# Kernel tuning notes

Hardware: AMD Instinct MI355X
Metric: run time of the kernel (lower is better)

## Reference

```python
import jax, jax.numpy as jnp
import numpy as np

B, J, H, W, P = 48, 17, 128, 128, 30  # batch, joints, heatmap HxW, max people
N = J * H * W  # flattened tag-map length per image


def setup_inputs() -> dict:
    key = jax.random.key(0)
    k1, k2, k3, k4 = jax.random.split(key, 4)
    outputs = jax.random.normal(k1, (B, 2 * J, H, W), dtype=jnp.float32)
    heatmaps = jax.random.uniform(k2, (B, J, H, W), dtype=jnp.float32)
    idx = jax.random.randint(k3, (B, P, J), 0, N)
    vis = jax.random.randint(k4, (B, P, J), 0, 2)
    joints = jnp.stack([idx, vis], axis=-1).astype(jnp.int64)  # [B,P,J,2]
    return {"outputs": outputs, "heatmaps": heatmaps, "joints": joints}


def _heatmap_mse(pred, gt):
    # mask over (batch, channel): channels whose gt sums to > 0
    mask = (gt.sum(axis=(2, 3)) > 0).astype(pred.dtype)  # [B,C]
    per = ((pred - gt) ** 2).mean(axis=(2, 3))            # [B,C]
    return (per * mask).sum() / mask.sum()


def _ae_loss(tags, joints):
    # tags: [B,N] flattened tag maps; joints: [B,P,J,2] int (idx, visibility)
    idx = joints[..., 0]
    vis = (joints[..., 1] > 0).astype(tags.dtype)         # [B,P,J]
    t = jax.vmap(lambda tg, ix: tg[ix])(tags, idx)        # [B,P,J] gathered tags
    cnt = vis.sum(-1)                                     # [B,P] visible joints per person
    person_valid = cnt > 0
    safe_cnt = jnp.where(person_valid, cnt, 1.0)
    m = (t * vis).sum(-1) / safe_cnt                      # [B,P] per-person mean tag
    per_pull = (vis * (t - m[..., None]) ** 2).sum(-1) / safe_cnt
    per_pull = jnp.where(person_valid, per_pull, 0.0)
    num_tags = person_valid.sum(-1).astype(tags.dtype)    # [B]
    pull = per_pull.sum(-1) / jnp.maximum(num_tags, 1.0)
    # push: all-pairs exp(-(m_i - m_j)^2) over valid persons, minus diagonal (num_tags)
    diff = m[:, :, None] - m[:, None, :]                  # [B,P,P]
    pair_mask = person_valid[:, :, None] & person_valid[:, None, :]
    push_raw = jnp.where(pair_mask, jnp.exp(-diff ** 2), 0.0).sum(axis=(1, 2)) - num_tags
    denom = (num_tags - 1.0) * num_tags
    push = jnp.where(num_tags >= 2.0,
                     push_raw / jnp.where(denom > 0, denom, 1.0) * 0.5,
                     0.0)
    return push, pull


def reference(outputs, heatmaps, joints):
    hm_pred = outputs[:, :J]                   # [B,J,H,W]
    tags = outputs[:, J:].reshape(B, -1)       # [B,N] (tag channels flattened)
    hm_loss = _heatmap_mse(hm_pred, heatmaps)  # scalar (factor 1.0)
    push, pull = _ae_loss(tags, joints)        # [B], [B] (factors 1.0)
    return hm_loss, push, pull
```

## Files before the change

### kernel.cpp

```cpp
#include <hip/hip_runtime.h>
#include <hip/hip_bf16.h>

constexpr int B = 48, J = 17, H = 128, W = 128, P = 30;
constexpr int HW = H * W;
constexpr int NPLANES = B * J;
constexpr int CHUNKS_PER_PLANE = 2;
constexpr int NCHUNK = NPLANES * CHUNKS_PER_PLANE;
constexpr int CHUNK_FLOATS = HW / CHUNKS_PER_PLANE;

__global__ __launch_bounds__(256) void fused_kernel(
        const float* __restrict__ outputs,
        const float* __restrict__ heatmaps,
        const unsigned* __restrict__ joints_u32,
        float* __restrict__ ws,
        float* __restrict__ out) {
    int t = threadIdx.x;

    if (blockIdx.x < NCHUNK) {
        int chunk = blockIdx.x;
        int plane = chunk >> 1, half = chunk & 1;
        int b = plane / J, j = plane % J;
        const float4* pred = reinterpret_cast<const float4*>(
            outputs + ((size_t)b * 2 * J + j) * HW + half * CHUNK_FLOATS);
        const float4* gt = reinterpret_cast<const float4*>(
            heatmaps + (size_t)plane * HW + half * CHUNK_FLOATS);

        float sq = 0.f, gs = 0.f;
#pragma unroll
        for (int k = 0; k < CHUNK_FLOATS / 4 / 256; ++k) {
            float4 p = pred[t + k * 256];
            float4 g = gt[t + k * 256];
            float d0 = p.x - g.x, d1 = p.y - g.y, d2 = p.z - g.z, d3 = p.w - g.w;
            sq += d0 * d0 + d1 * d1 + d2 * d2 + d3 * d3;
            gs += g.x + g.y + g.z + g.w;
        }
        for (int off = 32; off > 0; off >>= 1) {
            sq += __shfl_xor(sq, off);
            gs += __shfl_xor(gs, off);
        }
        __shared__ float s_sq[4], s_gs[4];
        int wave = t >> 6;
        if ((t & 63) == 0) { s_sq[wave] = sq; s_gs[wave] = gs; }
        __syncthreads();
        if (t == 0) {
            ws[2 * chunk]     = s_sq[0] + s_sq[1] + s_sq[2] + s_sq[3];
            ws[2 * chunk + 1] = s_gs[0] + s_gs[1] + s_gs[2] + s_gs[3];
        }
        return;
    }

    int b = blockIdx.x - NCHUNK;
    const float* tags = outputs + ((size_t)b * 2 * J + J) * HW;

    const unsigned* jw = joints_u32 + (size_t)b * P * J * 2 * 2;
    unsigned ob = 0;
#pragma unroll
    for (int k = 0; k < 4; ++k) {
        int i = t + k * 256;
        if (i < P * J * 2) ob |= jw[2 * i + 1];
    }
    __shared__ unsigned s_ob[4];
    for (int off = 32; off > 0; off >>= 1) ob |= (unsigned)__shfl_xor((int)ob, off);
    int wv = t >> 6;
    if ((t & 63) == 0) s_ob[wv] = ob;
    __shared__ float m_sh[P];
    __shared__ int v_sh[P];
    __syncthreads();
    bool is64 = (s_ob[0] | s_ob[1] | s_ob[2] | s_ob[3]) == 0u;

    if (t >= 64) return;
    int lane = t;

    float per_pull = 0.f, m = 0.f;
    int validp = 0;

    if (lane < P) {
        float tv[J];
        int   vv[J];
        int cnt = 0;
        float sum = 0.f;
        if (is64) {
            const long long* jp = reinterpret_cast<const long long*>(joints_u32)
                                  + ((size_t)b * P + lane) * J * 2;
#pragma unroll
            for (int j = 0; j < J; ++j) {
                int idx = (int)jp[2 * j];
                int vis = jp[2 * j + 1] > 0;
                float tval = tags[idx];
                tv[j] = tval; vv[j] = vis;
                cnt += vis;
                sum += vis ? tval : 0.f;
            }
        } else {
            const int* jp = reinterpret_cast<const int*>(joints_u32)
                            + ((size_t)b * P + lane) * J * 2;
#pragma unroll
            for (int j = 0; j < J; ++j) {
                int idx = jp[2 * j];
                int vis = jp[2 * j + 1] > 0;
                float tval = tags[idx];
                tv[j] = tval; vv[j] = vis;
                cnt += vis;
                sum += vis ? tval : 0.f;
            }
        }
        float safe = cnt > 0 ? (float)cnt : 1.f;
        m = sum / safe;
        float pp = 0.f;
#pragma unroll
        for (int j = 0; j < J; ++j) {
            float d = tv[j] - m;
            pp += vv[j] ? d * d : 0.f;
        }
        validp = (cnt > 0) ? 1 : 0;
        per_pull = validp ? pp / safe : 0.f;
        m_sh[lane] = m;
        v_sh[lane] = validp;
    }
    __builtin_amdgcn_s_waitcnt(0);

    float push_p = 0.f;
    if (lane < P && validp) {
#pragma unroll
        for (int k = 0; k < P; ++k) {
            if (v_sh[k]) {
                float d = m - m_sh[k];
                push_p += __expf(-d * d);
            }
        }
    }

    float v0 = per_pull, v1 = push_p, v2 = (float)validp;
    for (int off = 32; off > 0; off >>= 1) {
        v0 += __shfl_xor(v0, off);
        v1 += __shfl_xor(v1, off);
        v2 += __shfl_xor(v2, off);
    }
    if (lane == 0) {
        float num_tags = v2;
        float pull = v0 / fmaxf(num_tags, 1.f);
        float push_raw = v1 - num_tags;
        float denom = (num_tags - 1.f) * num_tags;
        float push = (num_tags >= 2.f) ? (push_raw / (denom > 0.f ? denom : 1.f)) * 0.5f : 0.f;
        out[1 + b] = push;
        out[1 + B + b] = pull;
    }
}

__global__ __launch_bounds__(256) void finalize_kernel(const float* __restrict__ ws,
                                                       float* __restrict__ out) {
    int t = threadIdx.x;
    float s = 0.f, c = 0.f;
    for (int p = t; p < NPLANES; p += 256) {
        int c0 = 2 * p, c1 = 2 * p + 1;
        float sq = ws[2 * c0] + ws[2 * c1];
        float gs = ws[2 * c0 + 1] + ws[2 * c1 + 1];
        bool mask = gs > 0.f;
        s += mask ? sq * (1.f / HW) : 0.f;
        c += mask ? 1.f : 0.f;
    }
    for (int off = 32; off > 0; off >>= 1) {
        s += __shfl_xor(s, off);
        c += __shfl_xor(c, off);
    }
    __shared__ float s_s[4], s_c[4];
    int wave = t >> 6;
    if ((t & 63) == 0) { s_s[wave] = s; s_c[wave] = c; }
    __syncthreads();
    if (t == 0) {
        out[0] = (s_s[0] + s_s[1] + s_s[2] + s_s[3]) /
                 (s_c[0] + s_c[1] + s_c[2] + s_c[3]);
    }
}

extern "C" void kernel_launch(void* const* d_in, const int* in_sizes, int n_in,
                              void* d_out, int out_size, void* d_ws, size_t ws_size,
                              hipStream_t stream) {
    const float* outputs  = (const float*)d_in[0];
    const float* heatmaps = (const float*)d_in[1];
    const unsigned* joints = (const unsigned*)d_in[2];
    float* out = (float*)d_out;
    float* ws  = (float*)d_ws;

    fused_kernel<<<NCHUNK + B, 256, 0, stream>>>(outputs, heatmaps, joints, ws, out);
    finalize_kernel<<<1, 256, 0, stream>>>(ws, out);
}
```

Baseline: 27.43 us.

## Replace finalize kernel with last-block atomic reduction and one block per plane

Measured after the change: 53.11 us. 1.94x slower.

```diff
diff --git a/kernel.cpp b/kernel.cpp
--- a/kernel.cpp
+++ b/kernel.cpp
@@ -4,30 +4,27 @@
 constexpr int B = 48, J = 17, H = 128, W = 128, P = 30;
 constexpr int HW = H * W;
 constexpr int NPLANES = B * J;
-constexpr int CHUNKS_PER_PLANE = 2;
-constexpr int NCHUNK = NPLANES * CHUNKS_PER_PLANE;
-constexpr int CHUNK_FLOATS = HW / CHUNKS_PER_PLANE;
+constexpr int AE_BLOCKS = B;
 
 __global__ __launch_bounds__(256) void fused_kernel(
         const float* __restrict__ outputs,
         const float* __restrict__ heatmaps,
         const unsigned* __restrict__ joints_u32,
-        float* __restrict__ ws,
+        unsigned long long* __restrict__ ws64,
         float* __restrict__ out) {
     int t = threadIdx.x;
 
-    if (blockIdx.x < NCHUNK) {
-        int chunk = blockIdx.x;
-        int plane = chunk >> 1, half = chunk & 1;
+    if (blockIdx.x >= AE_BLOCKS) {
+        int plane = blockIdx.x - AE_BLOCKS;
         int b = plane / J, j = plane % J;
         const float4* pred = reinterpret_cast<const float4*>(
-            outputs + ((size_t)b * 2 * J + j) * HW + half * CHUNK_FLOATS);
+            outputs + ((size_t)b * 2 * J + j) * HW);
         const float4* gt = reinterpret_cast<const float4*>(
-            heatmaps + (size_t)plane * HW + half * CHUNK_FLOATS);
+            heatmaps + (size_t)plane * HW);
 
         float sq = 0.f, gs = 0.f;
 #pragma unroll
-        for (int k = 0; k < CHUNK_FLOATS / 4 / 256; ++k) {
+        for (int k = 0; k < 16; ++k) {
             float4 p = pred[t + k * 256];
             float4 g = gt[t + k * 256];
             float d0 = p.x - g.x, d1 = p.y - g.y, d2 = p.z - g.z, d3 = p.w - g.w;
@@ -43,13 +40,28 @@
         if ((t & 63) == 0) { s_sq[wave] = sq; s_gs[wave] = gs; }
         __syncthreads();
         if (t == 0) {
-            ws[2 * chunk]     = s_sq[0] + s_sq[1] + s_sq[2] + s_sq[3];
-            ws[2 * chunk + 1] = s_gs[0] + s_gs[1] + s_gs[2] + s_gs[3];
+            float tot_sq = s_sq[0] + s_sq[1] + s_sq[2] + s_sq[3];
+            float tot_gs = s_gs[0] + s_gs[1] + s_gs[2] + s_gs[3];
+            unsigned* ws32 = reinterpret_cast<unsigned*>(ws64);
+            if (tot_gs > 0.f) {
+                unsigned long long fx = (unsigned long long)
+                    __double2ll_rn((double)tot_sq * 262144.0);
+                atomicAdd(ws64, fx);
+                atomicAdd(ws32 + 2, 1u);
+            }
+            __threadfence();
+            unsigned ticket = atomicAdd(ws32 + 3, 1u);
+            if (ticket == NPLANES - 1) {
+                __threadfence();
+                unsigned long long acc = atomicAdd(ws64, 0ull);
+                unsigned cnt = atomicAdd(ws32 + 2, 0u);
+                out[0] = (float)((double)acc * (1.0 / 4294967296.0) / (double)cnt);
+            }
         }
         return;
     }
 
-    int b = blockIdx.x - NCHUNK;
+    int b = blockIdx.x;
     const float* tags = outputs + ((size_t)b * 2 * J + J) * HW;
 
     const unsigned* jw = joints_u32 + (size_t)b * P * J * 2 * 2;
@@ -147,32 +159,6 @@
     }
 }
 
-__global__ __launch_bounds__(256) void finalize_kernel(const float* __restrict__ ws,
-                                                       float* __restrict__ out) {
-    int t = threadIdx.x;
-    float s = 0.f, c = 0.f;
-    for (int p = t; p < NPLANES; p += 256) {
-        int c0 = 2 * p, c1 = 2 * p + 1;
-        float sq = ws[2 * c0] + ws[2 * c1];
-        float gs = ws[2 * c0 + 1] + ws[2 * c1 + 1];
-        bool mask = gs > 0.f;
-        s += mask ? sq * (1.f / HW) : 0.f;
-        c += mask ? 1.f : 0.f;
-    }
-    for (int off = 32; off > 0; off >>= 1) {
-        s += __shfl_xor(s, off);
-        c += __shfl_xor(c, off);
-    }
-    __shared__ float s_s[4], s_c[4];
-    int wave = t >> 6;
-    if ((t & 63) == 0) { s_s[wave] = s; s_c[wave] = c; }
-    __syncthreads();
-    if (t == 0) {
-        out[0] = (s_s[0] + s_s[1] + s_s[2] + s_s[3]) /
-                 (s_c[0] + s_c[1] + s_c[2] + s_c[3]);
-    }
-}
-
 extern "C" void kernel_launch(void* const* d_in, const int* in_sizes, int n_in,
                               void* d_out, int out_size, void* d_ws, size_t ws_size,
                               hipStream_t stream) {
@@ -180,8 +166,9 @@
     const float* heatmaps = (const float*)d_in[1];
     const unsigned* joints = (const unsigned*)d_in[2];
     float* out = (float*)d_out;
-    float* ws  = (float*)d_ws;
 
-    fused_kernel<<<NCHUNK + B, 256, 0, stream>>>(outputs, heatmaps, joints, ws, out);
-    finalize_kernel<<<1, 256, 0, stream>>>(ws, out);
+    hipMemsetAsync(d_ws, 0, 16, stream);
+    fused_kernel<<<AE_BLOCKS + NPLANES, 256, 0, stream>>>(
+        outputs, heatmaps, joints,
+        reinterpret_cast<unsigned long long*>(d_ws), out);
 }
```
